# Kernel optimization log

Measured on AMD Instinct MI355X. Metric: run time of the kernel, lower is better.

## Reference

```python
import jax, jax.numpy as jnp
import numpy as np

EPS = 1e-6
NQ, NKV, D, HID = 40, 8, 128, 5120
QKV_DIM = (NQ + 2 * NKV) * D + NQ  # gating enabled


def rmsnorm(x, w):
    xf = x.astype(jnp.float32)
    n = jax.lax.rsqrt(jnp.mean(xf * xf, axis=-1, keepdims=True) + EPS)
    return (xf * n).astype(x.dtype) * w


def rope(x, cos, sin):
    # x: [B,S,h,d], cos/sin: [B,S,d]
    d = x.shape[-1]
    c = cos[..., None, :d]
    s = sin[..., None, :d]
    x1, x2 = x[..., : d // 2], x[..., d // 2 :]
    rot = jnp.concatenate([-x2, x1], axis=-1)
    return x * c + rot * s


def setup_inputs() -> dict:
    key = jax.random.key(0)
    ks = jax.random.split(key, 8)
    B, S = 1, 2048
    return {
        "x": jax.random.normal(ks[0], (B, S, HID), jnp.float32),
        "rope_cos": jax.random.normal(ks[1], (B, S, D), jnp.float32),
        "rope_sin": jax.random.normal(ks[2], (B, S, D), jnp.float32),
        "w_pre_norm": jnp.ones((HID,), jnp.float32),
        "w_qkv": jax.random.normal(ks[3], (HID, QKV_DIM), jnp.float32) * 0.02,
        "w_q_norm": jnp.ones((D,), jnp.float32),
        "w_k_norm": jnp.ones((D,), jnp.float32),
        "w_proj": jax.random.normal(ks[4], (NQ * D, HID), jnp.float32) * 0.02,
    }


def reference(x, rope_cos, rope_sin, w_pre_norm, w_qkv, w_q_norm, w_k_norm, w_proj):
    B, S, _ = x.shape
    normed = rmsnorm(x, w_pre_norm)
    qkv = normed @ w_qkv  # [B,S,QKV_DIM]
    q_dim, k_dim = NQ * D, NKV * D
    q = qkv[..., :q_dim].reshape(B, S, NQ, D)
    k = qkv[..., q_dim : q_dim + k_dim].reshape(B, S, NKV, D)
    v = qkv[..., q_dim + k_dim : q_dim + 2 * k_dim].reshape(B, S, NKV, D)
    gate = jax.nn.sigmoid(qkv[..., q_dim + 2 * k_dim :])  # [B,S,NQ]
    q = rmsnorm(q, w_q_norm)
    k = rmsnorm(k, w_k_norm)
    q = rope(q, rope_cos, rope_sin)
    k = rope(k, rope_cos, rope_sin)
    # GQA: expand kv groups to query heads
    rep = NQ // NKV
    k = jnp.repeat(k, rep, axis=2)  # [B,S,NQ,D]
    v = jnp.repeat(v, rep, axis=2)
    scale = 1.0 / jnp.sqrt(jnp.float32(D))
    scores = jnp.einsum("bqhd,bkhd->bhqk", q, k) * scale
    attn = jax.nn.softmax(scores, axis=-1)
    out = jnp.einsum("bhqk,bkhd->bqhd", attn, v)  # [B,S,NQ,D]
    out = out * gate[..., None]
    out = out.reshape(B, S, NQ * D)
    return out @ w_proj
```

## Files before the change

kernel.cpp:

```cpp
#include <hip/hip_runtime.h>
#include <hip/hip_bf16.h>
#include <stdint.h>

#define S_LEN 2048
#define NQh   40
#define NKVh  8
#define HD    128
#define HIDd  5120
#define QKV_C 7208
#define QKV_P 7424
#define NROW  (S_LEN * NQh)

typedef unsigned short u16;
typedef short bf16x8 __attribute__((ext_vector_type(8)));
typedef float f32x4  __attribute__((ext_vector_type(4)));
typedef u16   u16x4  __attribute__((ext_vector_type(4)));

typedef const __attribute__((address_space(1))) void* gas_ptr;
typedef __attribute__((address_space(3))) void*       las_ptr;

#define MFMA16(a, b, c) __builtin_amdgcn_mfma_f32_16x16x32_bf16(a, b, c, 0, 0, 0)

__device__ __forceinline__ u16 f2bf(float f) {
  union { float f; unsigned u; } v; v.f = f;
  return (u16)((v.u + 0x7fffu + ((v.u >> 16) & 1u)) >> 16);
}
__device__ __forceinline__ u16 f2bf_c(float f) {
  union { __hip_bfloat16 b; u16 u; } v;
  v.b = __float2bfloat16(f);
  return v.u;
}
__device__ __forceinline__ float b2f(u16 b) {
  union { unsigned u; float f; } v; v.u = ((unsigned)b) << 16; return v.f;
}

__device__ __forceinline__ float wave_sum64(float x) {
#pragma unroll
  for (int m = 32; m > 0; m >>= 1) x += __shfl_xor(x, m, 64);
  return x;
}

__device__ __forceinline__ void cstore(float* cp, long strideN, const f32x4& v) {
#pragma unroll
  for (int r = 0; r < 4; ++r) cp[(long)r * strideN] = v[r];
}
__device__ __forceinline__ void cstore(u16* cp, long strideN, const f32x4& v) {
#pragma unroll
  for (int r = 0; r < 4; ++r) cp[(long)r * strideN] = f2bf_c(v[r]);
}

__global__ __launch_bounds__(256) void prenorm_kernel(
    const float* __restrict__ x, const float* __restrict__ w, u16* __restrict__ xn) {
  int row = blockIdx.x;
  const float4* xr = (const float4*)(x + (size_t)row * HIDd);
  const float4* wr = (const float4*)w;
  float4 vx[5];
  float ss = 0.f;
#pragma unroll
  for (int c = 0; c < 5; ++c) {
    int i = c * 256 + threadIdx.x;
    vx[c] = xr[i];
    ss += vx[c].x * vx[c].x + vx[c].y * vx[c].y + vx[c].z * vx[c].z + vx[c].w * vx[c].w;
  }
  ss = wave_sum64(ss);
  __shared__ float red[4];
  if ((threadIdx.x & 63) == 0) red[threadIdx.x >> 6] = ss;
  __syncthreads();
  float tot = red[0] + red[1] + red[2] + red[3];
  float n = rsqrtf(tot * (1.f / HIDd) + 1e-6f);
  u16x4* out = (u16x4*)(xn + (size_t)row * HIDd);
#pragma unroll
  for (int c = 0; c < 5; ++c) {
    int i = c * 256 + threadIdx.x;
    float4 vw = wr[i];
    u16x4 o;
    o.x = f2bf(vx[c].x * n * vw.x);
    o.y = f2bf(vx[c].y * n * vw.y);
    o.z = f2bf(vx[c].z * n * vw.z);
    o.w = f2bf(vx[c].w * n * vw.w);
    out[i] = o;
  }
}

__global__ __launch_bounds__(256) void transpose_cvt(
    const float* __restrict__ src, u16* __restrict__ dst,
    int C, long ld_src, long ld_dst, long srcZ, long dstZ) {
  src += (long)blockIdx.z * srcZ;
  dst += (long)blockIdx.z * dstZ;
  __shared__ float t[32][34];
  int c0 = blockIdx.x * 32, r0 = blockIdx.y * 32;
  {
    int lc = threadIdx.x & 15, lr = threadIdx.x >> 4;
#pragma unroll
    for (int i = 0; i < 32; i += 16) {
      int r = r0 + lr + i;
      int c = c0 + lc * 2;
      float2 v = make_float2(0.f, 0.f);
      if (c < C) v = *(const float2*)(src + (long)r * ld_src + c);
      *(float2*)&t[lr + i][lc * 2] = v;
    }
  }
  __syncthreads();
  {
    int cc = threadIdx.x >> 3;
    int rq = (threadIdx.x & 7) * 4;
    int c = c0 + cc;
    if (c < C) {
      u16x4 o;
#pragma unroll
      for (int rr = 0; rr < 4; ++rr) o[rr] = f2bf(t[rq + rr][cc]);
      *(u16x4*)(dst + (long)c * ld_dst + (r0 + rq)) = o;
    }
  }
}

__global__ __launch_bounds__(256) void transpose_bf16(
    const u16* __restrict__ src, u16* __restrict__ dst,
    long ld_src, long ld_dst, long srcZ, long dstZ) {
  src += (long)blockIdx.z * srcZ;
  dst += (long)blockIdx.z * dstZ;
  __shared__ u16 t[32][34];
  int c0 = blockIdx.x * 32, r0 = blockIdx.y * 32;
  {
    int lc = threadIdx.x & 15, lr = threadIdx.x >> 4;
#pragma unroll
    for (int i = 0; i < 32; i += 16)
      *(unsigned*)&t[lr + i][lc * 2] =
          *(const unsigned*)(src + (long)(r0 + lr + i) * ld_src + c0 + lc * 2);
  }
  __syncthreads();
  {
    int cc = threadIdx.x >> 3;
    int rq = (threadIdx.x & 7) * 4;
    u16x4 o;
#pragma unroll
    for (int rr = 0; rr < 4; ++rr) o[rr] = t[rq + rr][cc];
    *(u16x4*)(dst + (long)(c0 + cc) * ld_dst + (r0 + rq)) = o;
  }
}

template<typename OutT>
__global__ __launch_bounds__(512, 1) void gemm8(
    const u16* __restrict__ A, const u16* __restrict__ BT, OutT* __restrict__ C,
    int M, int N, int K) {
  __shared__ __align__(16) char AL[65536];
  __shared__ __align__(16) char BL[65536];

  int tid = threadIdx.x, w = tid >> 6, l = tid & 63;
  int wm = w >> 2, wn = w & 3;
  int g = l >> 4, q = l & 15;

  int nwg = gridDim.x * gridDim.y;
  int wgid = blockIdx.y * gridDim.x + blockIdx.x;
  int cpx = nwg >> 3;
  int swz = (wgid & 7) * cpx + (wgid >> 3);
  int bx = swz % gridDim.x, by = swz / gridDim.x;
  long mBase = (long)by * 256, nBase = (long)bx * 256;
  long Kb = (long)K * 2;
  const char* Ag = (const char*)A + mBase * Kb;
  const char* Bg = (const char*)BT + nBase * Kb;

  int d0 = tid * 16, d1 = 8192 + tid * 16;
  long soff0 = (long)(d0 >> 6) * Kb + ((d0 & 63) ^ (((d0 >> 7) & 3) << 4));
  long soff1 = (long)(d1 >> 6) * Kb + ((d1 & 63) ^ (((d1 >> 7) & 3) << 4));

#define STG1(GBASE, LDSB, BUF, KH, T_)                                          \
  do {                                                                          \
    long kb_ = (long)(T_) * 128 + (KH) * 64;                                    \
    __builtin_amdgcn_global_load_lds((gas_ptr)((GBASE) + soff0 + kb_),          \
        (las_ptr)((LDSB) + (BUF) * 32768 + (KH) * 16384 + d0), 16, 0, 0);       \
    __builtin_amdgcn_global_load_lds((gas_ptr)((GBASE) + soff1 + kb_),          \
        (las_ptr)((LDSB) + (BUF) * 32768 + (KH) * 16384 + d1), 16, 0, 0);       \
  } while (0)

#define BARR                                                                    \
  do {                                                                          \
    __builtin_amdgcn_s_barrier();                                               \
    __builtin_amdgcn_sched_barrier(0);                                          \
  } while (0)
#define VMW(NLIT)                                                               \
  do {                                                                          \
    asm volatile("s_waitcnt vmcnt(" #NLIT ")" ::: "memory");                    \
    __builtin_amdgcn_sched_barrier(0);                                          \
  } while (0)

  int offA[8], offB[4];
#pragma unroll
  for (int i = 0; i < 8; ++i) {
    int r = wm * 128 + i * 16 + q;
    offA[i] = r * 64 + ((g * 16) ^ (((r >> 1) & 3) << 4));
  }
#pragma unroll
  for (int j = 0; j < 4; ++j) {
    int r = wn * 64 + j * 16 + q;
    offB[j] = r * 64 + ((g * 16) ^ (((r >> 1) & 3) << 4));
  }

#define RD_ALL(ABASE, BBASE)                                                    \
  do {                                                                          \
    _Pragma("unroll") for (int ii = 0; ii < 8; ++ii)                            \
      af[ii] = *(const bf16x8*)((ABASE) + offA[ii]);                            \
    _Pragma("unroll") for (int j = 0; j < 4; ++j)                               \
      bfr[j] = *(const bf16x8*)((BBASE) + offB[j]);                             \
  } while (0)
#define MFMA_ALL                                                                \
  do {                                                                          \
    __builtin_amdgcn_s_setprio(1);                                              \
    _Pragma("unroll") for (int ii = 0; ii < 8; ++ii)                            \
      _Pragma("unroll") for (int j = 0; j < 4; ++j)                             \
        acc[ii][j] = MFMA16(af[ii], bfr[j], acc[ii][j]);                        \
    __builtin_amdgcn_s_setprio(0);                                              \
  } while (0)

  f32x4 acc[8][4] = {};
  int NT = K >> 6;

  STG1(Ag, AL, 0, 0, 0); STG1(Bg, BL, 0, 0, 0);
  STG1(Ag, AL, 0, 1, 0); STG1(Bg, BL, 0, 1, 0);
  STG1(Ag, AL, 1, 0, 1); STG1(Bg, BL, 1, 0, 1);
  VMW(8); BARR;

  for (int t = 0; t < NT; ++t) {
    int buf = t & 1, nb = buf ^ 1;
    const char* Abuf = AL + buf * 32768;
    const char* Bbuf = BL + buf * 32768;
    bf16x8 af[8], bfr[4];

    RD_ALL(Abuf, Bbuf);
    if (t + 1 < NT) { STG1(Ag, AL, nb, 1, t + 1); STG1(Bg, BL, nb, 1, t + 1); }
    MFMA_ALL;
    if (t + 1 < NT) { VMW(8); } else { VMW(0); }
    BARR;

    RD_ALL(Abuf + 16384, Bbuf + 16384);
    if (t + 2 < NT) { STG1(Ag, AL, buf, 0, t + 2); STG1(Bg, BL, buf, 0, t + 2); }
    MFMA_ALL;
    if (t + 2 < NT)      { VMW(8); }
    else if (t + 1 < NT) { VMW(4); }
    BARR;
  }
#undef STG1
#undef RD_ALL
#undef MFMA_ALL
#undef BARR
#undef VMW

#pragma unroll
  for (int i = 0; i < 8; ++i)
#pragma unroll
    for (int j = 0; j < 4; ++j) {
      long mrow = mBase + wm * 128 + i * 16 + g * 4;
      long ncol = nBase + wn * 64 + j * 16 + q;
      cstore(C + mrow * N + ncol, N, acc[i][j]);
    }
}

__global__ __launch_bounds__(256) void split_kernel(
    const u16* __restrict__ qkv, const float* __restrict__ cosb,
    const float* __restrict__ sinb, const float* __restrict__ wq,
    const float* __restrict__ wk, u16* __restrict__ qb, u16* __restrict__ kb,
    float* __restrict__ gate) {
  int s = blockIdx.x;
  int w = threadIdx.x >> 6, l = threadIdx.x & 63;
  const u16* row = qkv + (size_t)s * QKV_P;
  float c0 = cosb[s * HD + l],      s0 = sinb[s * HD + l];
  float c1 = cosb[s * HD + 64 + l], s1 = sinb[s * HD + 64 + l];
  const float SCALE = 0.12751743f;
  for (int h = w; h < NQh; h += 4) {
    float x0 = b2f(row[h * HD + l]), x1 = b2f(row[h * HD + 64 + l]);
    float ss = wave_sum64(x0 * x0 + x1 * x1);
    float n = rsqrtf(ss * (1.f / HD) + 1e-6f);
    x0 *= n * wq[l]; x1 *= n * wq[64 + l];
    qb[((size_t)s * NQh + h) * HD + l]      = f2bf((x0 * c0 - x1 * s0) * SCALE);
    qb[((size_t)s * NQh + h) * HD + 64 + l] = f2bf((x1 * c1 + x0 * s1) * SCALE);
  }
  for (int h = w; h < NKVh; h += 4) {
    float x0 = b2f(row[NQh * HD + h * HD + l]), x1 = b2f(row[NQh * HD + h * HD + 64 + l]);
    float ss = wave_sum64(x0 * x0 + x1 * x1);
    float n = rsqrtf(ss * (1.f / HD) + 1e-6f);
    x0 *= n * wk[l]; x1 *= n * wk[64 + l];
    kb[((size_t)h * S_LEN + s) * HD + l]      = f2bf(x0 * c0 - x1 * s0);
    kb[((size_t)h * S_LEN + s) * HD + 64 + l] = f2bf(x1 * c1 + x0 * s1);
  }
  if (threadIdx.x < NQh) {
    float gx = b2f(row[(NQh + 2 * NKVh) * HD + threadIdx.x]);
    gate[(size_t)s * NQh + threadIdx.x] = 1.f / (1.f + expf(-gx));
  }
}

__global__ __launch_bounds__(256) void attn_kernel(
    const u16* __restrict__ qb, const u16* __restrict__ kb,
    const u16* __restrict__ vT,
    u16* __restrict__ opart, float* __restrict__ lpart) {
  int L = blockIdx.x;
  int xcd = L & 7, t0 = L >> 3;
  int G = xcd * 10 + (t0 >> 4);
  int bx = t0 & 15;
  int h = G % NQh, z = G / NQh;
  int hk = h / 5;
  int w = threadIdx.x >> 6, l = threadIdx.x & 63;
  int g = l >> 4, q = l & 15;
  int s0 = bx * 128 + w * 32;
  int tid = threadIdx.x;

  __shared__ __align__(16) u16 Ks[2][32 * 128];
  __shared__ __align__(16) u16 Vs[2][128 * 32];
  __shared__ __align__(16) u16 Plds[4][2][16][40];

  bf16x8 ones;
#pragma unroll
  for (int j = 0; j < 8; ++j) ones[j] = (short)0x3F80;

  bf16x8 qf[2][4];
#pragma unroll
  for (int p = 0; p < 2; ++p)
#pragma unroll
    for (int kk = 0; kk < 4; ++kk)
      qf[p][kk] = *(const bf16x8*)(qb + ((size_t)(s0 + p * 16 + q) * NQh + h) * HD + kk * 32 + g * 8);

  const char* KhB = (const char*)(kb + ((size_t)hk * S_LEN + z * 1024) * HD);
  const char* VhB = (const char*)(vT + (size_t)hk * HD * S_LEN + z * 1024);

  int Dk0 = tid * 16, Dk1 = 4096 + tid * 16;
  long ks0 = (long)(Dk0 >> 8) * 256 + ((Dk0 & 255) ^ (((Dk0 >> 8) & 7) << 4));
  long ks1 = (long)(Dk1 >> 8) * 256 + ((Dk1 & 255) ^ (((Dk1 >> 8) & 7) << 4));
  long vs0 = (long)(Dk0 >> 6) * 4096 + ((Dk0 & 63) ^ (((Dk0 >> 7) & 3) << 4));
  long vs1 = (long)(Dk1 >> 6) * 4096 + ((Dk1 & 63) ^ (((Dk1 >> 7) & 3) << 4));

#define STG(BUF, T_)                                                            \
  do {                                                                          \
    __builtin_amdgcn_global_load_lds((gas_ptr)(KhB + (long)(T_) * 8192 + ks0),  \
        (las_ptr)((char*)&Ks[BUF][0] + Dk0), 16, 0, 0);                         \
    __builtin_amdgcn_global_load_lds((gas_ptr)(KhB + (long)(T_) * 8192 + ks1),  \
        (las_ptr)((char*)&Ks[BUF][0] + Dk1), 16, 0, 0);                         \
    __builtin_amdgcn_global_load_lds((gas_ptr)(VhB + (long)(T_) * 64 + vs0),    \
        (las_ptr)((char*)&Vs[BUF][0] + Dk0), 16, 0, 0);                         \
    __builtin_amdgcn_global_load_lds((gas_ptr)(VhB + (long)(T_) * 64 + vs1),    \
        (las_ptr)((char*)&Vs[BUF][0] + Dk1), 16, 0, 0);                         \
  } while (0)

#define BARR                                                                    \
  do {                                                                          \
    __builtin_amdgcn_sched_barrier(0);                                          \
    __builtin_amdgcn_s_barrier();                                               \
    __builtin_amdgcn_sched_barrier(0);                                          \
  } while (0)

  f32x4 oacc[8][2] = {};
  f32x4 lacc[2] = {};
  int xq = (q & 7) << 4;
  int xv = ((q >> 1) & 3) << 4;

  STG(0, 0); STG(1, 1);
  __builtin_amdgcn_sched_barrier(0);
  asm volatile("s_waitcnt vmcnt(4)" ::: "memory");
  BARR;

  for (int step = 0; step < 32; ++step) {
    const char* kc = (const char*)&Ks[step & 1][0];
    const char* vc = (const char*)&Vs[step & 1][0];

    f32x4 sacc[2][2] = {};
#pragma unroll
    for (int kk = 0; kk < 4; ++kk) {
#pragma unroll
      for (int kt = 0; kt < 2; ++kt) {
        bf16x8 kf = *(const bf16x8*)(kc + (kt * 16 + q) * 256 + ((kk * 64 + g * 16) ^ xq));
        sacc[kt][0] = MFMA16(kf, qf[0][kk], sacc[kt][0]);
        sacc[kt][1] = MFMA16(kf, qf[1][kk], sacc[kt][1]);
      }
    }
    bf16x8 va[8];
#pragma unroll
    for (int dt = 0; dt < 8; ++dt)
      va[dt] = *(const bf16x8*)(vc + (dt * 16 + q) * 64 + ((g * 16) ^ xv));

#pragma unroll
    for (int p = 0; p < 2; ++p) {
#pragma unroll
      for (int kt = 0; kt < 2; ++kt) {
        u16x4 pk;
#pragma unroll
        for (int r = 0; r < 4; ++r) pk[r] = f2bf_c(exp2f(sacc[kt][p][r]));
        *(u16x4*)&Plds[w][p][q][kt * 16 + g * 4] = pk;
      }
    }
    bf16x8 pf0 = *(const bf16x8*)&Plds[w][0][q][g * 8];
    bf16x8 pf1 = *(const bf16x8*)&Plds[w][1][q][g * 8];
    __builtin_amdgcn_s_setprio(1);
#pragma unroll
    for (int dt = 0; dt < 8; ++dt) {
      oacc[dt][0] = MFMA16(va[dt], pf0, oacc[dt][0]);
      oacc[dt][1] = MFMA16(va[dt], pf1, oacc[dt][1]);
    }
    lacc[0] = MFMA16(ones, pf0, lacc[0]);
    lacc[1] = MFMA16(ones, pf1, lacc[1]);
    __builtin_amdgcn_s_setprio(0);

    BARR;
    if (step + 2 < 32) {
      STG(step & 1, step + 2);
      __builtin_amdgcn_sched_barrier(0);
      asm volatile("s_waitcnt vmcnt(4)" ::: "memory");
      __builtin_amdgcn_sched_barrier(0);
    } else if (step + 1 < 32) {
      __builtin_amdgcn_sched_barrier(0);
      asm volatile("s_waitcnt vmcnt(0)" ::: "memory");
      __builtin_amdgcn_sched_barrier(0);
    }
    BARR;
  }
#undef STG
#undef BARR

#pragma unroll
  for (int p = 0; p < 2; ++p) {
    size_t row = (size_t)(s0 + p * 16 + q) * NQh + h;
    if (g == 0) lpart[(size_t)z * NROW + row] = lacc[p][0];
    u16* op = opart + ((size_t)z * NROW + row) * HD;
#pragma unroll
    for (int dt = 0; dt < 8; ++dt) {
      u16x4 o;
#pragma unroll
      for (int r = 0; r < 4; ++r) o[r] = f2bf_c(oacc[dt][p][r]);
      *(u16x4*)(op + dt * 16 + g * 4) = o;
    }
  }
}

__global__ __launch_bounds__(256) void combine_kernel(
    const u16* __restrict__ opart, const float* __restrict__ lpart,
    const float* __restrict__ gate, u16* __restrict__ ob) {
  int t = blockIdx.x * 256 + threadIdx.x;
  int row = t >> 5, dv = (t & 31) * 4;
  float l0 = lpart[row], l1 = lpart[NROW + row];
  float sc = gate[row] / (l0 + l1);
  u16x4 o0 = *(const u16x4*)(opart + (size_t)row * HD + dv);
  u16x4 o1 = *(const u16x4*)(opart + (size_t)NROW * HD + (size_t)row * HD + dv);
  u16x4 o;
#pragma unroll
  for (int r = 0; r < 4; ++r) o[r] = f2bf(sc * (b2f(o0[r]) + b2f(o1[r])));
  *(u16x4*)(ob + (size_t)row * HD + dv) = o;
}

extern "C" void kernel_launch(void* const* d_in, const int* in_sizes, int n_in,
                              void* d_out, int out_size, void* d_ws, size_t ws_size,
                              hipStream_t stream) {
  const float* x     = (const float*)d_in[0];
  const float* rc    = (const float*)d_in[1];
  const float* rs    = (const float*)d_in[2];
  const float* wpre  = (const float*)d_in[3];
  const float* wqkv  = (const float*)d_in[4];
  const float* wqn   = (const float*)d_in[5];
  const float* wkn   = (const float*)d_in[6];
  const float* wproj = (const float*)d_in[7];
  float* out = (float*)d_out;

  char* ws = (char*)d_ws;
  size_t off = 0;
  auto alloc = [&](size_t bytes) -> void* {
    void* p = ws + off;
    off += (bytes + 255) & ~(size_t)255;
    return p;
  };
  u16*   xn     = (u16*)  alloc((size_t)S_LEN * HIDd * 2);
  u16*   wqkvT  = (u16*)  alloc((size_t)QKV_P * HIDd * 2);
  u16*   wprojT = (u16*)  alloc((size_t)HIDd * HIDd * 2);
  u16*   qkvb   = (u16*)  alloc((size_t)S_LEN * QKV_P * 2);
  u16*   qb     = (u16*)  alloc((size_t)S_LEN * NQh * HD * 2);
  u16*   kb     = (u16*)  alloc((size_t)NKVh * S_LEN * HD * 2);
  u16*   vT     = (u16*)  alloc((size_t)NKVh * HD * S_LEN * 2);
  float* gate   = (float*)alloc((size_t)S_LEN * NQh * 4);
  u16*   ob     = (u16*)  alloc((size_t)S_LEN * NQh * HD * 2);
  if (off > ws_size) return;

  u16*   opart = (u16*)ws;
  float* lpart = (float*)(opart + (size_t)2 * NROW * HD);

  prenorm_kernel<<<S_LEN, 256, 0, stream>>>(x, wpre, xn);
  transpose_cvt<<<dim3(QKV_P / 32, HIDd / 32, 1), 256, 0, stream>>>(
      wqkv, wqkvT, QKV_C, (long)QKV_C, (long)HIDd, 0, 0);
  transpose_cvt<<<dim3(HIDd / 32, HIDd / 32, 1), 256, 0, stream>>>(
      wproj, wprojT, HIDd, (long)HIDd, (long)HIDd, 0, 0);
  gemm8<u16><<<dim3(QKV_P / 256, S_LEN / 256), 512, 0, stream>>>(
      xn, wqkvT, qkvb, S_LEN, QKV_P, HIDd);
  split_kernel<<<S_LEN, 256, 0, stream>>>(qkvb, rc, rs, wqn, wkn, qb, kb, gate);
  transpose_bf16<<<dim3(HD / 32, S_LEN / 32, NKVh), 256, 0, stream>>>(
      qkvb + (NQh + NKVh) * HD, vT, (long)QKV_P, (long)S_LEN,
      128, (long)HD * S_LEN);
  attn_kernel<<<1280, 256, 0, stream>>>(qb, kb, vT, opart, lpart);
  combine_kernel<<<NROW * 32 / 256, 256, 0, stream>>>(
      opart, lpart, gate, ob);
  gemm8<float><<<dim3(HIDd / 256, S_LEN / 256), 512, 0, stream>>>(
      ob, wprojT, out, S_LEN, HIDd, HIDd);
}
```

Measured before the change: 571.8 us.

## Restructure GEMM main loop into 4-stage LDS ring with register double-buffered fragments

Result: no change. 570.5 us, median of 2 (-0.2%).

```diff
diff --git a/kernel.cpp b/kernel.cpp
--- a/kernel.cpp
+++ b/kernel.cpp
@@ -143,8 +143,8 @@
 __global__ __launch_bounds__(512, 1) void gemm8(
     const u16* __restrict__ A, const u16* __restrict__ BT, OutT* __restrict__ C,
     int M, int N, int K) {
-  __shared__ __align__(16) char AL[65536];
-  __shared__ __align__(16) char BL[65536];
+  __shared__ __align__(16) char AL[4 * 16384];
+  __shared__ __align__(16) char BL[4 * 16384];
 
   int tid = threadIdx.x, w = tid >> 6, l = tid & 63;
   int wm = w >> 2, wn = w & 3;
@@ -164,23 +164,31 @@
   long soff0 = (long)(d0 >> 6) * Kb + ((d0 & 63) ^ (((d0 >> 7) & 3) << 4));
   long soff1 = (long)(d1 >> 6) * Kb + ((d1 & 63) ^ (((d1 >> 7) & 3) << 4));
 
-#define STG1(GBASE, LDSB, BUF, KH, T_)                                          \
-  do {                                                                          \
-    long kb_ = (long)(T_) * 128 + (KH) * 64;                                    \
-    __builtin_amdgcn_global_load_lds((gas_ptr)((GBASE) + soff0 + kb_),          \
-        (las_ptr)((LDSB) + (BUF) * 32768 + (KH) * 16384 + d0), 16, 0, 0);       \
-    __builtin_amdgcn_global_load_lds((gas_ptr)((GBASE) + soff1 + kb_),          \
-        (las_ptr)((LDSB) + (BUF) * 32768 + (KH) * 16384 + d1), 16, 0, 0);       \
-  } while (0)
-
-#define BARR                                                                    \
-  do {                                                                          \
+#define STG(J)                                                                  \
+  do {                                                                          \
+    long kb_ = (long)(J) * 64;                                                  \
+    char* la_ = AL + ((J) & 3) * 16384;                                         \
+    char* lb_ = BL + ((J) & 3) * 16384;                                         \
+    __builtin_amdgcn_global_load_lds((gas_ptr)(Ag + soff0 + kb_),               \
+        (las_ptr)(la_ + d0), 16, 0, 0);                                         \
+    __builtin_amdgcn_global_load_lds((gas_ptr)(Ag + soff1 + kb_),               \
+        (las_ptr)(la_ + d1), 16, 0, 0);                                         \
+    __builtin_amdgcn_global_load_lds((gas_ptr)(Bg + soff0 + kb_),               \
+        (las_ptr)(lb_ + d0), 16, 0, 0);                                         \
+    __builtin_amdgcn_global_load_lds((gas_ptr)(Bg + soff1 + kb_),               \
+        (las_ptr)(lb_ + d1), 16, 0, 0);                                         \
+  } while (0)
+
+#define VMW(NLIT)                                                               \
+  do {                                                                          \
+    asm volatile("s_waitcnt vmcnt(" #NLIT ")" ::: "memory");                    \
+    __builtin_amdgcn_sched_barrier(0);                                          \
+  } while (0)
+#define LKW_BARR                                                                \
+  do {                                                                          \
+    asm volatile("s_waitcnt lgkmcnt(0)" ::: "memory");                          \
+    __builtin_amdgcn_sched_barrier(0);                                          \
     __builtin_amdgcn_s_barrier();                                               \
-    __builtin_amdgcn_sched_barrier(0);                                          \
-  } while (0)
-#define VMW(NLIT)                                                               \
-  do {                                                                          \
-    asm volatile("s_waitcnt vmcnt(" #NLIT ")" ::: "memory");                    \
     __builtin_amdgcn_sched_barrier(0);                                          \
   } while (0)
 
@@ -196,54 +204,58 @@
     offB[j] = r * 64 + ((g * 16) ^ (((r >> 1) & 3) << 4));
   }
 
-#define RD_ALL(ABASE, BBASE)                                                    \
-  do {                                                                          \
+#define RD(J, AF, BF)                                                           \
+  do {                                                                          \
+    const char* ab_ = AL + ((J) & 3) * 16384;                                   \
+    const char* bb_ = BL + ((J) & 3) * 16384;                                   \
     _Pragma("unroll") for (int ii = 0; ii < 8; ++ii)                            \
-      af[ii] = *(const bf16x8*)((ABASE) + offA[ii]);                            \
+      AF[ii] = *(const bf16x8*)(ab_ + offA[ii]);                                \
     _Pragma("unroll") for (int j = 0; j < 4; ++j)                               \
-      bfr[j] = *(const bf16x8*)((BBASE) + offB[j]);                             \
-  } while (0)
-#define MFMA_ALL                                                                \
+      BF[j] = *(const bf16x8*)(bb_ + offB[j]);                                  \
+  } while (0)
+#define MM(AF, BF)                                                              \
   do {                                                                          \
     __builtin_amdgcn_s_setprio(1);                                              \
     _Pragma("unroll") for (int ii = 0; ii < 8; ++ii)                            \
       _Pragma("unroll") for (int j = 0; j < 4; ++j)                             \
-        acc[ii][j] = MFMA16(af[ii], bfr[j], acc[ii][j]);                        \
+        acc[ii][j] = MFMA16(AF[ii], BF[j], acc[ii][j]);                         \
     __builtin_amdgcn_s_setprio(0);                                              \
   } while (0)
 
+#define PHASE(I, CA, CB, NA, NB)                                                \
+  do {                                                                          \
+    int i_ = (I);                                                               \
+    if (i_ + 1 < NP) RD(i_ + 1, NA, NB);                                        \
+    if (i_ + 4 < NP) STG(i_ + 4);                                               \
+    MM(CA, CB);                                                                 \
+    if (i_ + 4 < NP)       { VMW(8); }                                          \
+    else if (i_ + 4 == NP) { VMW(4); }                                          \
+    else if (i_ + 3 == NP) { VMW(0); }                                          \
+    LKW_BARR;                                                                   \
+  } while (0)
+
   f32x4 acc[8][4] = {};
-  int NT = K >> 6;
-
-  STG1(Ag, AL, 0, 0, 0); STG1(Bg, BL, 0, 0, 0);
-  STG1(Ag, AL, 0, 1, 0); STG1(Bg, BL, 0, 1, 0);
-  STG1(Ag, AL, 1, 0, 1); STG1(Bg, BL, 1, 0, 1);
-  VMW(8); BARR;
-
-  for (int t = 0; t < NT; ++t) {
-    int buf = t & 1, nb = buf ^ 1;
-    const char* Abuf = AL + buf * 32768;
-    const char* Bbuf = BL + buf * 32768;
-    bf16x8 af[8], bfr[4];
-
-    RD_ALL(Abuf, Bbuf);
-    if (t + 1 < NT) { STG1(Ag, AL, nb, 1, t + 1); STG1(Bg, BL, nb, 1, t + 1); }
-    MFMA_ALL;
-    if (t + 1 < NT) { VMW(8); } else { VMW(0); }
-    BARR;
-
-    RD_ALL(Abuf + 16384, Bbuf + 16384);
-    if (t + 2 < NT) { STG1(Ag, AL, buf, 0, t + 2); STG1(Bg, BL, buf, 0, t + 2); }
-    MFMA_ALL;
-    if (t + 2 < NT)      { VMW(8); }
-    else if (t + 1 < NT) { VMW(4); }
-    BARR;
-  }
-#undef STG1
-#undef RD_ALL
-#undef MFMA_ALL
-#undef BARR
+  int NP = K >> 5;
+
+  bf16x8 afA[8], bfA[4], afB[8], bfB[4];
+
+  STG(0); STG(1); STG(2); STG(3);
+  VMW(8);
+  __builtin_amdgcn_s_barrier();
+  __builtin_amdgcn_sched_barrier(0);
+  RD(0, afA, bfA);
+  LKW_BARR;
+
+  for (int i = 0; i < NP; i += 2) {
+    PHASE(i,     afA, bfA, afB, bfB);
+    PHASE(i + 1, afB, bfB, afA, bfA);
+  }
+#undef STG
+#undef RD
+#undef MM
+#undef PHASE
 #undef VMW
+#undef LKW_BARR
 
 #pragma unroll
   for (int i = 0; i < 8; ++i)
```
